# Optimization experiments

Hardware: AMD Instinct MI355X
Metric: run time of the kernel (lower is better)

The kernel has to match this reference:

```python
import jax, jax.numpy as jnp
import numpy as np

B, L, D, H, NB = 8, 256, 128, 4, 2
HD = D // H
N_ITEMS, TIME_SPAN = 50000, 256
EPS = 1e-8
NEG = -(2.0 ** 32) + 1.0  # torch uses -2**32+1 padding value


def _ln(x, g, b):
    m = jnp.mean(x, -1, keepdims=True)
    v = jnp.mean((x - m) ** 2, -1, keepdims=True)
    return (x - m) / jnp.sqrt(v + EPS) * g + b


def setup_inputs() -> dict:
    ks = iter(jax.random.split(jax.random.key(0), 40))

    def nrm(shape, s=0.02):
        return jax.random.normal(next(ks), shape, jnp.float32) * s

    inp = {
        "user_ids": jax.random.randint(next(ks), (B,), 0, 1000),
        "log_seqs": jax.random.randint(next(ks), (B, L), 0, N_ITEMS + 1),
        "time_matrices": jax.random.randint(next(ks), (B, L, L), 0, TIME_SPAN + 1),
        "pos_seqs": jax.random.randint(next(ks), (B, L), 1, N_ITEMS + 1),
        "neg_seqs": jax.random.randint(next(ks), (B, L), 1, N_ITEMS + 1),
    }
    inp["item_emb"] = nrm((N_ITEMS + 1, D)).at[0].set(0.0)  # padding_idx=0
    inp["posK_emb"] = nrm((L, D))
    inp["posV_emb"] = nrm((L, D))
    inp["timeK_emb"] = nrm((TIME_SPAN + 1, D))
    inp["timeV_emb"] = nrm((TIME_SPAN + 1, D))
    inp["ln1_g"] = jnp.ones((NB, D)); inp["ln1_b"] = jnp.zeros((NB, D))
    inp["Wq"] = nrm((NB, D, D)); inp["bq"] = jnp.zeros((NB, D))
    inp["Wk"] = nrm((NB, D, D)); inp["bk"] = jnp.zeros((NB, D))
    inp["Wv"] = nrm((NB, D, D)); inp["bv"] = jnp.zeros((NB, D))
    inp["ln2_g"] = jnp.ones((NB, D)); inp["ln2_b"] = jnp.zeros((NB, D))
    inp["W1"] = nrm((NB, D, D)); inp["b1"] = jnp.zeros((NB, D))
    inp["W2"] = nrm((NB, D, D)); inp["b2"] = jnp.zeros((NB, D))
    inp["lnf_g"] = jnp.ones((D,)); inp["lnf_b"] = jnp.zeros((D,))
    return inp


def reference(user_ids, log_seqs, time_matrices, pos_seqs, neg_seqs,
              item_emb, posK_emb, posV_emb, timeK_emb, timeV_emb,
              ln1_g, ln1_b, Wq, bq, Wk, bk, Wv, bv, ln2_g, ln2_b,
              W1, b1, W2, b2, lnf_g, lnf_b):
    # dropout layers are identity in eval mode
    seqs = item_emb[log_seqs] * jnp.sqrt(jnp.float32(D))          # [B,L,D]
    tK = timeK_emb[time_matrices].reshape(B, L, L, H, HD)          # [B,Lq,Lk,H,hd]
    tV = timeV_emb[time_matrices].reshape(B, L, L, H, HD)
    pad = log_seqs == 0                                            # [B,L]
    seqs = seqs * (~pad)[..., None]
    causal = jnp.triu(jnp.ones((L, L), bool), 1)                   # ~tril -> masked
    # time_mask masks by QUERY position (matches torch unsqueeze(-1).expand)
    mask = pad[:, None, :, None] | causal[None, None]              # [B,1,Lq,Lk]
    posKh = posK_emb.reshape(L, H, HD)
    posVh = posV_emb.reshape(L, H, HD)
    for i in range(NB):
        q_in = _ln(seqs, ln1_g[i], ln1_b[i])
        Qh = (q_in @ Wq[i] + bq[i]).reshape(B, L, H, HD).transpose(0, 2, 1, 3)
        Kh = (seqs @ Wk[i] + bk[i]).reshape(B, L, H, HD).transpose(0, 2, 1, 3)
        Vh = (seqs @ Wv[i] + bv[i]).reshape(B, L, H, HD).transpose(0, 2, 1, 3)
        scores = jnp.einsum("bhqd,bhkd->bhqk", Qh, Kh)
        scores = scores + jnp.einsum("bhqd,khd->bhqk", Qh, posKh)
        scores = scores + jnp.einsum("bqkhd,bhqd->bhqk", tK, Qh)
        scores = scores / jnp.sqrt(jnp.float32(HD))
        scores = jnp.where(mask, NEG, scores)
        A = jax.nn.softmax(scores, axis=-1)                        # [B,H,Lq,Lk]
        out = jnp.einsum("bhqk,bhkd->bhqd", A, Vh)
        out = out + jnp.einsum("bhqk,khd->bhqd", A, posVh)
        out = out + jnp.einsum("bhqk,bqkhd->bhqd", A, tV)
        out = out.transpose(0, 2, 1, 3).reshape(B, L, D)
        seqs = q_in + out                                          # residual on Q
        seqs = _ln(seqs, ln2_g[i], ln2_b[i])
        h = jax.nn.relu(seqs @ W1[i] + b1[i])                      # conv1d k=1 == linear
        seqs = seqs + (h @ W2[i] + b2[i])
        seqs = seqs * (~pad)[..., None]
    feats = _ln(seqs, lnf_g, lnf_b)
    pos_logits = jnp.sum(feats * item_emb[pos_seqs], -1)           # [B,L]
    neg_logits = jnp.sum(feats * item_emb[neg_seqs], -1)
    return (pos_logits, neg_logits)
```

## Files before the change

kernel.cpp:

```cpp
#include <hip/hip_runtime.h>
#include <hip/hip_bf16.h>

#define L_ 256
#define H_ 4
#define ROWS 2048
#define NEGV (-4294967295.0f)

typedef unsigned short us16;

__device__ __forceinline__ float us2f(us16 u){ return __uint_as_float(((unsigned)u)<<16); }
__device__ __forceinline__ us16 f2us(float f){ __hip_bfloat16 h=__float2bfloat16(f); return *(us16*)&h; }

struct KArgs {
    const int *log_seqs, *tmat, *pos_seqs, *neg_seqs;
    const float *item_emb, *posK, *posV, *timeK, *timeV;
    const float *ln1g, *ln1b, *bq, *bk, *bv, *ln2g, *ln2b, *b1, *b2, *lnfg, *lnfb;
    const float *Wq, *Wk, *Wv, *W1, *W2;
    float *qin0, *qin1, *out;
    us16 *wsW, *tmK, *tmV, *Qb0, *Kb0, *Vb0, *Qb1, *Kb1, *Vb1;
};

__device__ __forceinline__ void stage_w(const us16* __restrict__ Wg, us16* sW, int tid){
    const uint4* src=(const uint4*)Wg;
    uint4* dst=(uint4*)sW;
    #pragma unroll
    for(int j=0;j<8;j++) dst[j*256+tid]=src[j*256+tid];
}

__device__ __forceinline__ void ln_rows(float* sA,
        const float* __restrict__ g, const float* __restrict__ b,
        float* qin_out, int r0, int tid){
    int r=tid>>5, l=tid&31;
    float* x=sA+r*128;
    float x0=x[l],x1=x[l+32],x2=x[l+64],x3=x[l+96];
    float s=x0+x1+x2+x3;
    #pragma unroll
    for(int o=16;o;o>>=1) s+=__shfl_xor(s,o,64);
    float m=s*(1.f/128.f);
    float d0=x0-m,d1=x1-m,d2=x2-m,d3=x3-m;
    float v=d0*d0+d1*d1+d2*d2+d3*d3;
    #pragma unroll
    for(int o=16;o;o>>=1) v+=__shfl_xor(v,o,64);
    float rstd=rsqrtf(v*(1.f/128.f)+1e-8f);
    float y0=d0*rstd*g[l]+b[l];
    float y1=d1*rstd*g[l+32]+b[l+32];
    float y2=d2*rstd*g[l+64]+b[l+64];
    float y3=d3*rstd*g[l+96]+b[l+96];
    x[l]=y0; x[l+32]=y1; x[l+64]=y2; x[l+96]=y3;
    if(qin_out){
        float* q=qin_out+(size_t)(r0+r)*128;
        q[l]=y0; q[l+32]=y1; q[l+64]=y2; q[l+96]=y3;
    }
}

__device__ __forceinline__ void gemm2x2(const float* A, const us16* sW,
        int ra, int rb, int c0, float* acc){
    float a00=0,a01=0,a10=0,a11=0;
    const float* Ar=A+ra*128;
    const float* Br=A+rb*128;
    #pragma unroll 8
    for(int k=0;k<128;k++){
        ushort2 wp=*(const ushort2*)(sW+k*128+c0);
        float w0=us2f(wp.x), w1=us2f(wp.y);
        float x0=Ar[k], x1=Br[k];
        a00=fmaf(x0,w0,a00); a01=fmaf(x0,w1,a01);
        a10=fmaf(x1,w0,a10); a11=fmaf(x1,w1,a11);
    }
    acc[0]=a00; acc[1]=a01; acc[2]=a10; acc[3]=a11;
}

__global__ __launch_bounds__(256) void k_pre(KArgs a){
    __shared__ __align__(16) char smem[36864];
    int tid=threadIdx.x, bid=blockIdx.x;
    if(bid<768){
        us16* sW=(us16*)smem;
        float* sA=(float*)(smem+32768);
        int m=bid>>8, rg=bid&255, r0=rg*8;
        {
            int rl=tid>>5, c4=tid&31;
            int id=a.log_seqs[r0+rl];
            float4 v=((const float4*)a.item_emb)[id*32+c4];
            float sc = id? 11.3137085f : 0.f;
            v.x*=sc; v.y*=sc; v.z*=sc; v.w*=sc;
            ((float4*)sA)[tid]=v;
        }
        const float* Wsrc=(m==0)?a.Wq:(m==1)?a.Wk:a.Wv;
        {
            const float4* src=(const float4*)Wsrc;
            ushort4* dst=(ushort4*)sW;
            #pragma unroll
            for(int j=0;j<16;j++){
                float4 w=src[j*256+tid];
                ushort4 o; o.x=f2us(w.x);o.y=f2us(w.y);o.z=f2us(w.z);o.w=f2us(w.w);
                dst[j*256+tid]=o;
            }
        }
        __syncthreads();
        if(m==0){ ln_rows(sA, a.ln1g, a.ln1b, a.qin0, r0, tid); __syncthreads(); }
        int cp=tid&63, rp=tid>>6, c0=2*cp, ra=2*rp, rb=ra+1;
        float acc[4];
        gemm2x2(sA,sW,ra,rb,c0,acc);
        if(m==0){
            float b0v=a.bq[c0], b1v=a.bq[c0+1];
            ushort2 s0; s0.x=f2us(acc[0]+b0v); s0.y=f2us(acc[1]+b1v);
            ushort2 s1; s1.x=f2us(acc[2]+b0v); s1.y=f2us(acc[3]+b1v);
            *(ushort2*)(a.Qb0+(size_t)(r0+ra)*128+c0)=s0;
            *(ushort2*)(a.Qb0+(size_t)(r0+rb)*128+c0)=s1;
        } else {
            const float* bb=(m==1)?a.bk:a.bv;
            const float* pp=(m==1)?a.posK:a.posV;
            us16* Oo=(m==1)?a.Kb0:a.Vb0;
            int qa=(r0+ra)&255, qb2=(r0+rb)&255;
            float b0v=bb[c0], b1v=bb[c0+1];
            ushort2 s0; s0.x=f2us(acc[0]+b0v+pp[qa*128+c0]);  s0.y=f2us(acc[1]+b1v+pp[qa*128+c0+1]);
            ushort2 s1; s1.x=f2us(acc[2]+b0v+pp[qb2*128+c0]); s1.y=f2us(acc[3]+b1v+pp[qb2*128+c0+1]);
            *(ushort2*)(Oo+(size_t)(r0+ra)*128+c0)=s0;
            *(ushort2*)(Oo+(size_t)(r0+rb)*128+c0)=s1;
        }
    } else if(bid<880){
        int j=bid-768; int m=j>>4; int idx=(j&15)*256+tid;
        const float* base;
        switch(m){
            case 0: base=a.W1; break;        case 1: base=a.W2; break;
            case 2: base=a.Wq+16384; break;  case 3: base=a.Wk+16384; break;
            case 4: base=a.Wv+16384; break;  case 5: base=a.W1+16384; break;
            default: base=a.W2+16384; break;
        }
        float4 v=((const float4*)base)[idx];
        ushort4 o; o.x=f2us(v.x);o.y=f2us(v.y);o.z=f2us(v.z);o.w=f2us(v.w);
        ((ushort4*)(a.wsW+(size_t)m*16384))[idx]=o;
    } else {
        int gi=(bid-880)*256+tid;
        if(gi<8224){
            float4 v=((const float4*)a.timeK)[gi];
            ushort4 o; o.x=f2us(v.x);o.y=f2us(v.y);o.z=f2us(v.z);o.w=f2us(v.w);
            ((ushort4*)a.tmK)[gi]=o;
        } else if(gi<16448){
            int g2=gi-8224;
            float4 v=((const float4*)a.timeV)[g2];
            ushort4 o; o.x=f2us(v.x);o.y=f2us(v.y);o.z=f2us(v.z);o.w=f2us(v.w);
            ((ushort4*)a.tmV)[g2]=o;
        }
    }
}

__global__ __launch_bounds__(256,4) void k_blk(KArgs a, int layer){
    __shared__ __align__(16) char smem[36864];
    float* sQ  =(float*)smem;
    float* sS  =(float*)(smem+1024);
    int*   sTM =(int*)  (smem+9216);
    float* sPr =(float*)(smem+11264);
    float* sRed=(float*)(smem+19456);
    float* sRed2=(float*)(smem+19472);
    us16*  sW  =(us16*) smem;
    float* sX  =(float*)(smem+32768);
    float* sH  =(float*)(smem+33792);
    float* sY  =(float*)(smem+34816);
    float* sRB =(float*)(smem+35840);

    int tid=threadIdx.x, bid=blockIdx.x;
    int b=bid>>7, p=bid&127;
    int q1=p, q2=255-p, b0=b*L_;
    int r1=b0+q1, r2=b0+q2;
    bool pad1=a.log_seqs[r1]==0, pad2=a.log_seqs[r2]==0;
    const us16* Qb = layer? a.Qb1:a.Qb0;
    const us16* Kb = layer? a.Kb1:a.Kb0;
    const us16* Vb = layer? a.Vb1:a.Vb0;
    const float* qin = layer? a.qin1:a.qin0;
    const float scale=0.17677669529663687f;
    if(tid<128) sQ[tid]=us2f(Qb[(size_t)r1*128+tid])*scale;
    else        sQ[tid]=us2f(Qb[(size_t)r2*128+(tid-128)])*scale;
    int k=tid;
    int tm1=a.tmat[(size_t)r1*L_+k], tm2=a.tmat[(size_t)r2*L_+k];
    sTM[k]=tm1; sTM[256+k]=tm2;
    __syncthreads();

    {
        const uint4* K4=(const uint4*)(Kb+(size_t)(b0+k)*128);
        #pragma unroll
        for(int i2=0;i2<2;i2++){
            int qq=i2?q2:q1; bool pad=i2?pad2:pad1;
            int tm=i2?tm2:tm1;
            bool act=(k<=qq)&&!pad;
            float acc[4]={0.f,0.f,0.f,0.f};
            if(act){
                const uint4* T4=(const uint4*)(a.tmK+(size_t)tm*128);
                const float4* Q4=(const float4*)(sQ+i2*128);
                #pragma unroll
                for(int c=0;c<16;c++){
                    uint4 kv=K4[c]; uint4 tv=T4[c];
                    float4 qa=Q4[2*c], qb=Q4[2*c+1];
                    const us16* ku=(const us16*)&kv;
                    const us16* tu=(const us16*)&tv;
                    acc[c>>2]+= qa.x*(us2f(ku[0])+us2f(tu[0]))
                              + qa.y*(us2f(ku[1])+us2f(tu[1]))
                              + qa.z*(us2f(ku[2])+us2f(tu[2]))
                              + qa.w*(us2f(ku[3])+us2f(tu[3]))
                              + qb.x*(us2f(ku[4])+us2f(tu[4]))
                              + qb.y*(us2f(ku[5])+us2f(tu[5]))
                              + qb.z*(us2f(ku[6])+us2f(tu[6]))
                              + qb.w*(us2f(ku[7])+us2f(tu[7]));
                }
            }
            #pragma unroll
            for(int h=0;h<H_;h++) sS[(i2*4+h)*256+k]= act? acc[h]:NEGV;
        }
    }
    __syncthreads();

    {
        int h=tid>>6, lane=tid&63;
        #pragma unroll
        for(int i2=0;i2<2;i2++){
            float* row=sS+(i2*4+h)*256;
            float v0=row[lane],v1=row[lane+64],v2=row[lane+128],v3=row[lane+192];
            float mm=fmaxf(fmaxf(v0,v1),fmaxf(v2,v3));
            #pragma unroll
            for(int o=32;o;o>>=1) mm=fmaxf(mm,__shfl_xor(mm,o,64));
            float e0=__expf(v0-mm),e1=__expf(v1-mm),e2=__expf(v2-mm),e3=__expf(v3-mm);
            float ss=e0+e1+e2+e3;
            #pragma unroll
            for(int o=32;o;o>>=1) ss+=__shfl_xor(ss,o,64);
            float inv=1.f/ss;
            row[lane]=e0*inv; row[lane+64]=e1*inv; row[lane+128]=e2*inv; row[lane+192]=e3*inv;
        }
    }
    __syncthreads();

    {
        int i2=tid>>7, s8=(tid>>4)&7, dq=tid&15;
        int qq=i2?q2:q1; bool pad=i2?pad2:pad1;
        int kend=pad?L_:qq+1;
        int k0=s8*32;
        int kmax=kend-k0; kmax=kmax<0?0:(kmax>32?32:kmax);
        const float* row=sS+(i2*4+(dq>>2))*256;
        const int* tmrow=sTM+i2*256;
        float a0=0,a1=0,a2=0,a3=0,a4=0,a5=0,a6=0,a7=0;
        for(int kk=0;kk<kmax;kk++){
            int kx=k0+kk;
            float aa=row[kx];
            int tmk=tmrow[kx];
            uint4 v4=((const uint4*)(Vb+(size_t)(b0+kx)*128))[dq];
            uint4 t4=((const uint4*)(a.tmV+(size_t)tmk*128))[dq];
            const us16* vu=(const us16*)&v4;
            const us16* tu=(const us16*)&t4;
            a0=fmaf(aa,us2f(vu[0])+us2f(tu[0]),a0);
            a1=fmaf(aa,us2f(vu[1])+us2f(tu[1]),a1);
            a2=fmaf(aa,us2f(vu[2])+us2f(tu[2]),a2);
            a3=fmaf(aa,us2f(vu[3])+us2f(tu[3]),a3);
            a4=fmaf(aa,us2f(vu[4])+us2f(tu[4]),a4);
            a5=fmaf(aa,us2f(vu[5])+us2f(tu[5]),a5);
            a6=fmaf(aa,us2f(vu[6])+us2f(tu[6]),a6);
            a7=fmaf(aa,us2f(vu[7])+us2f(tu[7]),a7);
        }
        float* dst=sPr+(i2*8+s8)*128+dq*8;
        ((float4*)dst)[0]=make_float4(a0,a1,a2,a3);
        ((float4*)dst)[1]=make_float4(a4,a5,a6,a7);
    }
    __syncthreads();

    int ii=tid>>7, l=tid&127;
    bool padown = ii? pad2:pad1;
    int rr = ii? r2:r1;
    int qown = ii? q2:q1;
    {
        float v=qin[(size_t)rr*128+l];
        #pragma unroll
        for(int sl=0;sl<8;sl++) v+=sPr[(ii*8+sl)*128+l];
        float s=v;
        #pragma unroll
        for(int o=32;o;o>>=1) s+=__shfl_xor(s,o,64);
        if((tid&63)==0) sRed[ii*2+((tid>>6)&1)]=s;
        __syncthreads();
        float m=(sRed[ii*2]+sRed[ii*2+1])*(1.f/128.f);
        float d=v-m;
        float vv=d*d;
        #pragma unroll
        for(int o=32;o;o>>=1) vv+=__shfl_xor(vv,o,64);
        if((tid&63)==0) sRed2[ii*2+((tid>>6)&1)]=vv;
        __syncthreads();
        float rstd=rsqrtf((sRed2[ii*2]+sRed2[ii*2+1])*(1.f/128.f)+1e-8f);
        float y=d*rstd*a.ln2g[layer*128+l]+a.ln2b[layer*128+l];
        __syncthreads();
        sX[ii*128+l]=y;
    }
    __syncthreads();

    int cc=l;
    stage_w(a.wsW+(size_t)(layer?5:0)*16384, sW, tid);
    __syncthreads();
    {
        const float* xr=sX+ii*128;
        float h=0;
        #pragma unroll 16
        for(int k2=0;k2<128;k2++) h=fmaf(xr[k2],us2f(sW[k2*128+cc]),h);
        h=fmaxf(h+a.b1[layer*128+cc],0.f);
        __syncthreads();
        sH[ii*128+cc]=h;
    }
    __syncthreads();
    stage_w(a.wsW+(size_t)(layer?6:1)*16384, sW, tid);
    __syncthreads();
    float f;
    {
        const float* hr=sH+ii*128;
        float acc=0;
        #pragma unroll 16
        for(int k2=0;k2<128;k2++) acc=fmaf(hr[k2],us2f(sW[k2*128+cc]),acc);
        f=acc+a.b2[layer*128+cc]+sX[ii*128+cc];
        if(padown) f=0.f;
    }
    __syncthreads();

    if(layer==0){
        sY[ii*128+cc]=f;
        float s=f;
        #pragma unroll
        for(int o=32;o;o>>=1) s+=__shfl_xor(s,o,64);
        if((tid&63)==0) sRB[ii*2+((tid>>6)&1)]=s;
        __syncthreads();
        float m=(sRB[ii*2]+sRB[ii*2+1])*(1.f/128.f);
        float d=f-m;
        float vv=d*d;
        #pragma unroll
        for(int o=32;o;o>>=1) vv+=__shfl_xor(vv,o,64);
        if((tid&63)==0) sRB[4+ii*2+((tid>>6)&1)]=vv;
        __syncthreads();
        float rstd=rsqrtf((sRB[4+ii*2]+sRB[5+ii*2])*(1.f/128.f)+1e-8f);
        float y1=d*rstd*a.ln1g[128+cc]+a.ln1b[128+cc];
        a.qin1[(size_t)rr*128+cc]=y1;
        sX[ii*128+cc]=y1;
        __syncthreads();
        stage_w(a.wsW+(size_t)2*16384, sW, tid);
        __syncthreads();
        {
            const float* xr=sX+ii*128;
            float acc=0;
            #pragma unroll 16
            for(int k2=0;k2<128;k2++) acc=fmaf(xr[k2],us2f(sW[k2*128+cc]),acc);
            acc+=a.bq[128+cc];
            a.Qb1[(size_t)rr*128+cc]=f2us(acc);
        }
        __syncthreads();
        stage_w(a.wsW+(size_t)3*16384, sW, tid);
        __syncthreads();
        {
            const float* yr=sY+ii*128;
            float acc=0;
            #pragma unroll 16
            for(int k2=0;k2<128;k2++) acc=fmaf(yr[k2],us2f(sW[k2*128+cc]),acc);
            acc+=a.bk[128+cc]+a.posK[qown*128+cc];
            a.Kb1[(size_t)rr*128+cc]=f2us(acc);
        }
        __syncthreads();
        stage_w(a.wsW+(size_t)4*16384, sW, tid);
        __syncthreads();
        {
            const float* yr=sY+ii*128;
            float acc=0;
            #pragma unroll 16
            for(int k2=0;k2<128;k2++) acc=fmaf(yr[k2],us2f(sW[k2*128+cc]),acc);
            acc+=a.bv[128+cc]+a.posV[qown*128+cc];
            a.Vb1[(size_t)rr*128+cc]=f2us(acc);
        }
    } else {
        float s=f;
        #pragma unroll
        for(int o=32;o;o>>=1) s+=__shfl_xor(s,o,64);
        if((tid&63)==0) sRB[ii*2+((tid>>6)&1)]=s;
        __syncthreads();
        float m=(sRB[ii*2]+sRB[ii*2+1])*(1.f/128.f);
        float d=f-m;
        float vv=d*d;
        #pragma unroll
        for(int o=32;o;o>>=1) vv+=__shfl_xor(vv,o,64);
        if((tid&63)==0) sRB[4+ii*2+((tid>>6)&1)]=vv;
        __syncthreads();
        float rstd=rsqrtf((sRB[4+ii*2]+sRB[5+ii*2])*(1.f/128.f)+1e-8f);
        sX[ii*128+cc]=d*rstd*a.lnfg[cc]+a.lnfb[cc];
        __syncthreads();
        int w=tid>>6, lane=tid&63;
        int rowi=w>>1, neg=w&1;
        int rg = rowi? r2:r1;
        int id = neg? a.neg_seqs[rg] : a.pos_seqs[rg];
        const float* e=a.item_emb+(size_t)id*128;
        float s2 = sX[rowi*128+lane]*e[lane] + sX[rowi*128+lane+64]*e[lane+64];
        #pragma unroll
        for(int o=32;o;o>>=1) s2+=__shfl_xor(s2,o,64);
        if(lane==0) a.out[neg*ROWS+rg]=s2;
    }
}

extern "C" void kernel_launch(void* const* d_in, const int* in_sizes, int n_in,
                              void* d_out, int out_size, void* d_ws, size_t ws_size,
                              hipStream_t stream) {
    KArgs a;
    a.log_seqs=(const int*)d_in[1];
    a.tmat    =(const int*)d_in[2];
    a.pos_seqs=(const int*)d_in[3];
    a.neg_seqs=(const int*)d_in[4];
    a.item_emb=(const float*)d_in[5];
    a.posK =(const float*)d_in[6];
    a.posV =(const float*)d_in[7];
    a.timeK=(const float*)d_in[8];
    a.timeV=(const float*)d_in[9];
    a.ln1g=(const float*)d_in[10];
    a.ln1b=(const float*)d_in[11];
    a.Wq=(const float*)d_in[12];
    a.bq=(const float*)d_in[13];
    a.Wk=(const float*)d_in[14];
    a.bk=(const float*)d_in[15];
    a.Wv=(const float*)d_in[16];
    a.bv=(const float*)d_in[17];
    a.ln2g=(const float*)d_in[18];
    a.ln2b=(const float*)d_in[19];
    a.W1=(const float*)d_in[20];
    a.b1=(const float*)d_in[21];
    a.W2=(const float*)d_in[22];
    a.b2=(const float*)d_in[23];
    a.lnfg=(const float*)d_in[24];
    a.lnfb=(const float*)d_in[25];

    const size_t MB=1u<<20;
    char* w=(char*)d_ws;
    a.qin0=(float*)(w+0*MB);
    a.qin1=(float*)(w+1*MB);
    a.Qb0 =(us16*) (w+2*MB);
    a.Kb0 =(us16*) (w+2*MB+512*1024);
    a.Vb0 =(us16*) (w+3*MB);
    a.Qb1 =(us16*) (w+3*MB+512*1024);
    a.Kb1 =(us16*) (w+4*MB);
    a.Vb1 =(us16*) (w+4*MB+512*1024);
    a.wsW =(us16*) (w+5*MB);
    a.tmK =(us16*) (w+5*MB+256*1024);
    a.tmV =(us16*) (w+5*MB+384*1024);
    a.out =(float*)d_out;

    k_pre<<<946,256,0,stream>>>(a);
    k_blk<<<1024,256,0,stream>>>(a,0);
    k_blk<<<1024,256,0,stream>>>(a,1);
}
```

Measured before the change: 212.8 us.

## Precompute Q·timeK table per query and read transposed weights directly from global

Rather than gathering a timeK row for every (q,k) pair, each block computes dot products of its two queries with all 257 time embeddings into a shared table, then looks up that table when building scores. This swaps 256 gathers per query for 257 dense dot products. The small MLP and QKV GEMVs now read weights pre-transposed into column-major bf16 straight from global/L2, with no staging through LDS, which removes several barriers. Shared memory drops to 32KB and launch bounds go to 5 blocks per CU. The transposed writes in the pre-kernel become scattered stores.

```diff
diff --git a/kernel.cpp b/kernel.cpp
--- a/kernel.cpp
+++ b/kernel.cpp
@@ -17,15 +17,8 @@
     const float *ln1g, *ln1b, *bq, *bk, *bv, *ln2g, *ln2b, *b1, *b2, *lnfg, *lnfb;
     const float *Wq, *Wk, *Wv, *W1, *W2;
     float *qin0, *qin1, *out;
-    us16 *wsW, *tmK, *tmV, *Qb0, *Kb0, *Vb0, *Qb1, *Kb1, *Vb1;
+    us16 *wsWT, *tmK, *tmV, *Qb0, *Kb0, *Vb0, *Qb1, *Kb1, *Vb1;
 };
-
-__device__ __forceinline__ void stage_w(const us16* __restrict__ Wg, us16* sW, int tid){
-    const uint4* src=(const uint4*)Wg;
-    uint4* dst=(uint4*)sW;
-    #pragma unroll
-    for(int j=0;j<8;j++) dst[j*256+tid]=src[j*256+tid];
-}
 
 __device__ __forceinline__ void ln_rows(float* sA,
         const float* __restrict__ g, const float* __restrict__ b,
@@ -69,6 +62,20 @@
     acc[0]=a00; acc[1]=a01; acc[2]=a10; acc[3]=a11;
 }
 
+__device__ __forceinline__ float gemv_wt(const us16* __restrict__ wt, const float* x){
+    float acc=0;
+    const uint4* W4=(const uint4*)wt;
+    #pragma unroll
+    for(int c=0;c<16;c++){
+        uint4 wv=W4[c];
+        const us16* wu=(const us16*)&wv;
+        const float* xx=x+c*8;
+        acc += xx[0]*us2f(wu[0])+xx[1]*us2f(wu[1])+xx[2]*us2f(wu[2])+xx[3]*us2f(wu[3])
+             + xx[4]*us2f(wu[4])+xx[5]*us2f(wu[5])+xx[6]*us2f(wu[6])+xx[7]*us2f(wu[7]);
+    }
+    return acc;
+}
+
 __global__ __launch_bounds__(256) void k_pre(KArgs a){
     __shared__ __align__(16) char smem[36864];
     int tid=threadIdx.x, bid=blockIdx.x;
@@ -127,8 +134,13 @@
             default: base=a.W2+16384; break;
         }
         float4 v=((const float4*)base)[idx];
-        ushort4 o; o.x=f2us(v.x);o.y=f2us(v.y);o.z=f2us(v.z);o.w=f2us(v.w);
-        ((ushort4*)(a.wsW+(size_t)m*16384))[idx]=o;
+        int kRow = idx>>5;
+        int c0 = (idx&31)*4;
+        us16* dst = a.wsWT + (size_t)m*16384;
+        dst[(size_t)(c0+0)*128 + kRow]=f2us(v.x);
+        dst[(size_t)(c0+1)*128 + kRow]=f2us(v.y);
+        dst[(size_t)(c0+2)*128 + kRow]=f2us(v.z);
+        dst[(size_t)(c0+3)*128 + kRow]=f2us(v.w);
     } else {
         int gi=(bid-880)*256+tid;
         if(gi<8224){
@@ -144,19 +156,19 @@
     }
 }
 
-__global__ __launch_bounds__(256,4) void k_blk(KArgs a, int layer){
-    __shared__ __align__(16) char smem[36864];
+__global__ __launch_bounds__(256,5) void k_blk(KArgs a, int layer){
+    __shared__ __align__(16) char smem[32768];
     float* sQ  =(float*)smem;
     float* sS  =(float*)(smem+1024);
     int*   sTM =(int*)  (smem+9216);
     float* sPr =(float*)(smem+11264);
-    float* sRed=(float*)(smem+19456);
-    float* sRed2=(float*)(smem+19472);
-    us16*  sW  =(us16*) smem;
-    float* sX  =(float*)(smem+32768);
-    float* sH  =(float*)(smem+33792);
-    float* sY  =(float*)(smem+34816);
-    float* sRB =(float*)(smem+35840);
+    float* sDQ =(float*)(smem+19456);
+    float* sRed=(float*)(smem+27680);
+    float* sRed2=(float*)(smem+27696);
+    float* sX  =(float*)(smem+28672);
+    float* sH  =(float*)(smem+29696);
+    float* sY  =(float*)(smem+30720);
+    float* sRB =(float*)(smem+31744);
 
     int tid=threadIdx.x, bid=blockIdx.x;
     int b=bid>>7, p=bid&127;
@@ -175,35 +187,47 @@
     sTM[k]=tm1; sTM[256+k]=tm2;
     __syncthreads();
 
+    for(int j=tid;j<514;j+=256){
+        int i2 = j>=257; int t = j - i2*257;
+        const uint4* T4=(const uint4*)(a.tmK+(size_t)t*128);
+        const float* Qs = sQ + i2*128;
+        float acc[4]={0.f,0.f,0.f,0.f};
+        #pragma unroll
+        for(int c=0;c<16;c++){
+            uint4 tv=T4[c];
+            const us16* tu=(const us16*)&tv;
+            const float* qq=Qs+c*8;
+            acc[c>>2] += qq[0]*us2f(tu[0])+qq[1]*us2f(tu[1])
+                       + qq[2]*us2f(tu[2])+qq[3]*us2f(tu[3])
+                       + qq[4]*us2f(tu[4])+qq[5]*us2f(tu[5])
+                       + qq[6]*us2f(tu[6])+qq[7]*us2f(tu[7]);
+        }
+        #pragma unroll
+        for(int h=0;h<H_;h++) sDQ[(i2*4+h)*257+t]=acc[h];
+    }
+    __syncthreads();
+
     {
         const uint4* K4=(const uint4*)(Kb+(size_t)(b0+k)*128);
-        #pragma unroll
-        for(int i2=0;i2<2;i2++){
-            int qq=i2?q2:q1; bool pad=i2?pad2:pad1;
-            int tm=i2?tm2:tm1;
-            bool act=(k<=qq)&&!pad;
-            float acc[4]={0.f,0.f,0.f,0.f};
-            if(act){
-                const uint4* T4=(const uint4*)(a.tmK+(size_t)tm*128);
-                const float4* Q4=(const float4*)(sQ+i2*128);
-                #pragma unroll
-                for(int c=0;c<16;c++){
-                    uint4 kv=K4[c]; uint4 tv=T4[c];
-                    float4 qa=Q4[2*c], qb=Q4[2*c+1];
-                    const us16* ku=(const us16*)&kv;
-                    const us16* tu=(const us16*)&tv;
-                    acc[c>>2]+= qa.x*(us2f(ku[0])+us2f(tu[0]))
-                              + qa.y*(us2f(ku[1])+us2f(tu[1]))
-                              + qa.z*(us2f(ku[2])+us2f(tu[2]))
-                              + qa.w*(us2f(ku[3])+us2f(tu[3]))
-                              + qb.x*(us2f(ku[4])+us2f(tu[4]))
-                              + qb.y*(us2f(ku[5])+us2f(tu[5]))
-                              + qb.z*(us2f(ku[6])+us2f(tu[6]))
-                              + qb.w*(us2f(ku[7])+us2f(tu[7]));
-                }
-            }
-            #pragma unroll
-            for(int h=0;h<H_;h++) sS[(i2*4+h)*256+k]= act? acc[h]:NEGV;
+        float accA[4]={0.f,0.f,0.f,0.f}, accB[4]={0.f,0.f,0.f,0.f};
+        #pragma unroll
+        for(int c=0;c<16;c++){
+            uint4 kv=K4[c];
+            const us16* ku=(const us16*)&kv;
+            float kf0=us2f(ku[0]),kf1=us2f(ku[1]),kf2=us2f(ku[2]),kf3=us2f(ku[3]);
+            float kf4=us2f(ku[4]),kf5=us2f(ku[5]),kf6=us2f(ku[6]),kf7=us2f(ku[7]);
+            const float* qa=sQ+c*8;
+            const float* qb=sQ+128+c*8;
+            accA[c>>2] += qa[0]*kf0+qa[1]*kf1+qa[2]*kf2+qa[3]*kf3
+                        + qa[4]*kf4+qa[5]*kf5+qa[6]*kf6+qa[7]*kf7;
+            accB[c>>2] += qb[0]*kf0+qb[1]*kf1+qb[2]*kf2+qb[3]*kf3
+                        + qb[4]*kf4+qb[5]*kf5+qb[6]*kf6+qb[7]*kf7;
+        }
+        bool act1=(k<=q1)&&!pad1, act2=(k<=q2)&&!pad2;
+        #pragma unroll
+        for(int h=0;h<H_;h++){
+            sS[h*256+k]     = act1? accA[h]+sDQ[h*257+tm1]     : NEGV;
+            sS[(4+h)*256+k] = act2? accB[h]+sDQ[(4+h)*257+tm2] : NEGV;
         }
     }
     __syncthreads();
@@ -280,37 +304,25 @@
         if((tid&63)==0) sRed2[ii*2+((tid>>6)&1)]=vv;
         __syncthreads();
         float rstd=rsqrtf((sRed2[ii*2]+sRed2[ii*2+1])*(1.f/128.f)+1e-8f);
-        float y=d*rstd*a.ln2g[layer*128+l]+a.ln2b[layer*128+l];
-        __syncthreads();
-        sX[ii*128+l]=y;
+        sX[ii*128+l]=d*rstd*a.ln2g[layer*128+l]+a.ln2b[layer*128+l];
     }
     __syncthreads();
 
     int cc=l;
-    stage_w(a.wsW+(size_t)(layer?5:0)*16384, sW, tid);
-    __syncthreads();
-    {
-        const float* xr=sX+ii*128;
-        float h=0;
-        #pragma unroll 16
-        for(int k2=0;k2<128;k2++) h=fmaf(xr[k2],us2f(sW[k2*128+cc]),h);
-        h=fmaxf(h+a.b1[layer*128+cc],0.f);
-        __syncthreads();
+    const us16* WT1 = a.wsWT + (size_t)(layer?5:0)*16384;
+    const us16* WT2 = a.wsWT + (size_t)(layer?6:1)*16384;
+    {
+        float h = gemv_wt(WT1 + (size_t)cc*128, sX+ii*128);
+        h = fmaxf(h + a.b1[layer*128+cc], 0.f);
         sH[ii*128+cc]=h;
     }
     __syncthreads();
-    stage_w(a.wsW+(size_t)(layer?6:1)*16384, sW, tid);
-    __syncthreads();
     float f;
     {
-        const float* hr=sH+ii*128;
-        float acc=0;
-        #pragma unroll 16
-        for(int k2=0;k2<128;k2++) acc=fmaf(hr[k2],us2f(sW[k2*128+cc]),acc);
-        f=acc+a.b2[layer*128+cc]+sX[ii*128+cc];
+        f = gemv_wt(WT2 + (size_t)cc*128, sH+ii*128)
+          + a.b2[layer*128+cc] + sX[ii*128+cc];
         if(padown) f=0.f;
     }
-    __syncthreads();
 
     if(layer==0){
         sY[ii*128+cc]=f;
@@ -331,37 +343,17 @@
         a.qin1[(size_t)rr*128+cc]=y1;
         sX[ii*128+cc]=y1;
         __syncthreads();
-        stage_w(a.wsW+(size_t)2*16384, sW, tid);
-        __syncthreads();
         {
-            const float* xr=sX+ii*128;
-            float acc=0;
-            #pragma unroll 16
-            for(int k2=0;k2<128;k2++) acc=fmaf(xr[k2],us2f(sW[k2*128+cc]),acc);
-            acc+=a.bq[128+cc];
-            a.Qb1[(size_t)rr*128+cc]=f2us(acc);
-        }
-        __syncthreads();
-        stage_w(a.wsW+(size_t)3*16384, sW, tid);
-        __syncthreads();
+            float acc = gemv_wt(a.wsWT + (size_t)2*16384 + (size_t)cc*128, sX+ii*128);
+            a.Qb1[(size_t)rr*128+cc]=f2us(acc + a.bq[128+cc]);
+        }
         {
-            const float* yr=sY+ii*128;
-            float acc=0;
-            #pragma unroll 16
-            for(int k2=0;k2<128;k2++) acc=fmaf(yr[k2],us2f(sW[k2*128+cc]),acc);
-            acc+=a.bk[128+cc]+a.posK[qown*128+cc];
-            a.Kb1[(size_t)rr*128+cc]=f2us(acc);
-        }
-        __syncthreads();
-        stage_w(a.wsW+(size_t)4*16384, sW, tid);
-        __syncthreads();
+            float acc = gemv_wt(a.wsWT + (size_t)3*16384 + (size_t)cc*128, sY+ii*128);
+            a.Kb1[(size_t)rr*128+cc]=f2us(acc + a.bk[128+cc] + a.posK[qown*128+cc]);
+        }
         {
-            const float* yr=sY+ii*128;
-            float acc=0;
-            #pragma unroll 16
-            for(int k2=0;k2<128;k2++) acc=fmaf(yr[k2],us2f(sW[k2*128+cc]),acc);
-            acc+=a.bv[128+cc]+a.posV[qown*128+cc];
-            a.Vb1[(size_t)rr*128+cc]=f2us(acc);
+            float acc = gemv_wt(a.wsWT + (size_t)4*16384 + (size_t)cc*128, sY+ii*128);
+            a.Vb1[(size_t)rr*128+cc]=f2us(acc + a.bv[128+cc] + a.posV[qown*128+cc]);
         }
     } else {
         float s=f;
@@ -431,7 +423,7 @@
     a.Qb1 =(us16*) (w+3*MB+512*1024);
     a.Kb1 =(us16*) (w+4*MB);
     a.Vb1 =(us16*) (w+4*MB+512*1024);
-    a.wsW =(us16*) (w+5*MB);
+    a.wsWT=(us16*) (w+5*MB);
     a.tmK =(us16*) (w+5*MB+256*1024);
     a.tmV =(us16*) (w+5*MB+384*1024);
     a.out =(float*)d_out;
```

New measurement: 406.0 us. 1.91x slower.

## Double k_blk threads to 512 and split work across query rows and K halves

Applied to the files above, without the earlier changes.

Each block of k_blk now runs 512 threads. The score phase gives each query row its own thread half, the AV phase splits keys into 16 slices, and each 128x128 GEMV splits its K dimension across two thread halves, with partial sums reduced through shared memory. Time indices are stored as 16-bit values to free shared memory. The aim is more parallelism and latency hiding per block. The cost is extra barriers, idle threads in the LayerNorm sections, and larger shared-memory use, which may reduce occupancy.

```diff
diff --git a/kernel.cpp b/kernel.cpp
--- a/kernel.cpp
+++ b/kernel.cpp
@@ -19,13 +19,6 @@
     float *qin0, *qin1, *out;
     us16 *wsW, *tmK, *tmV, *Qb0, *Kb0, *Vb0, *Qb1, *Kb1, *Vb1;
 };
-
-__device__ __forceinline__ void stage_w(const us16* __restrict__ Wg, us16* sW, int tid){
-    const uint4* src=(const uint4*)Wg;
-    uint4* dst=(uint4*)sW;
-    #pragma unroll
-    for(int j=0;j<8;j++) dst[j*256+tid]=src[j*256+tid];
-}
 
 __device__ __forceinline__ void ln_rows(float* sA,
         const float* __restrict__ g, const float* __restrict__ b,
@@ -144,19 +137,36 @@
     }
 }
 
-__global__ __launch_bounds__(256,4) void k_blk(KArgs a, int layer){
-    __shared__ __align__(16) char smem[36864];
+__device__ __forceinline__ void stage_w512(const us16* __restrict__ Wg, us16* sW, int tid){
+    const uint4* src=(const uint4*)Wg;
+    uint4* dst=(uint4*)sW;
+    #pragma unroll
+    for(int j=0;j<4;j++) dst[j*512+tid]=src[j*512+tid];
+}
+
+__device__ __forceinline__ float gemv_half(const us16* sW, const float* x, int kh, int cc){
+    float acc=0;
+    int k0=kh*64;
+    #pragma unroll 16
+    for(int j=0;j<64;j++)
+        acc=fmaf(x[k0+j], us2f(sW[(size_t)(k0+j)*128+cc]), acc);
+    return acc;
+}
+
+__global__ __launch_bounds__(512,6) void k_blk(KArgs a, int layer){
+    __shared__ __align__(16) char smem[38912];
     float* sQ  =(float*)smem;
     float* sS  =(float*)(smem+1024);
-    int*   sTM =(int*)  (smem+9216);
-    float* sPr =(float*)(smem+11264);
-    float* sRed=(float*)(smem+19456);
-    float* sRed2=(float*)(smem+19472);
-    us16*  sW  =(us16*) smem;
+    us16*  sTMu=(us16*)(smem+9216);
+    float* sPr =(float*)(smem+10240);
+    float* sRed=(float*)(smem+26624);
+    float* sRed2=(float*)(smem+26640);
+    us16*  sW  =(us16*)smem;
     float* sX  =(float*)(smem+32768);
     float* sH  =(float*)(smem+33792);
     float* sY  =(float*)(smem+34816);
-    float* sRB =(float*)(smem+35840);
+    float* sPart=(float*)(smem+35840);
+    float* sRB =(float*)(smem+37888);
 
     int tid=threadIdx.x, bid=blockIdx.x;
     int b=bid>>7, p=bid&127;
@@ -168,73 +178,69 @@
     const us16* Vb = layer? a.Vb1:a.Vb0;
     const float* qin = layer? a.qin1:a.qin0;
     const float scale=0.17677669529663687f;
-    if(tid<128) sQ[tid]=us2f(Qb[(size_t)r1*128+tid])*scale;
-    else        sQ[tid]=us2f(Qb[(size_t)r2*128+(tid-128)])*scale;
-    int k=tid;
-    int tm1=a.tmat[(size_t)r1*L_+k], tm2=a.tmat[(size_t)r2*L_+k];
-    sTM[k]=tm1; sTM[256+k]=tm2;
+    if(tid<256){
+        int i2=tid>>7, l=tid&127;
+        sQ[tid]=us2f(Qb[(size_t)(i2?r2:r1)*128+l])*scale;
+    }
+    int i2g=tid>>8, kg=tid&255;
+    int rg_ = i2g? r2:r1;
+    int tmg = a.tmat[(size_t)rg_*L_+kg];
+    sTMu[i2g*256+kg]=(us16)tmg;
     __syncthreads();
 
     {
-        const uint4* K4=(const uint4*)(Kb+(size_t)(b0+k)*128);
-        #pragma unroll
-        for(int i2=0;i2<2;i2++){
-            int qq=i2?q2:q1; bool pad=i2?pad2:pad1;
-            int tm=i2?tm2:tm1;
-            bool act=(k<=qq)&&!pad;
-            float acc[4]={0.f,0.f,0.f,0.f};
-            if(act){
-                const uint4* T4=(const uint4*)(a.tmK+(size_t)tm*128);
-                const float4* Q4=(const float4*)(sQ+i2*128);
-                #pragma unroll
-                for(int c=0;c<16;c++){
-                    uint4 kv=K4[c]; uint4 tv=T4[c];
-                    float4 qa=Q4[2*c], qb=Q4[2*c+1];
-                    const us16* ku=(const us16*)&kv;
-                    const us16* tu=(const us16*)&tv;
-                    acc[c>>2]+= qa.x*(us2f(ku[0])+us2f(tu[0]))
-                              + qa.y*(us2f(ku[1])+us2f(tu[1]))
-                              + qa.z*(us2f(ku[2])+us2f(tu[2]))
-                              + qa.w*(us2f(ku[3])+us2f(tu[3]))
-                              + qb.x*(us2f(ku[4])+us2f(tu[4]))
-                              + qb.y*(us2f(ku[5])+us2f(tu[5]))
-                              + qb.z*(us2f(ku[6])+us2f(tu[6]))
-                              + qb.w*(us2f(ku[7])+us2f(tu[7]));
-                }
+        int qq = i2g? q2:q1; bool pad = i2g? pad2:pad1;
+        bool act=(kg<=qq)&&!pad;
+        float acc[4]={0.f,0.f,0.f,0.f};
+        if(act){
+            const uint4* K4=(const uint4*)(Kb+(size_t)(b0+kg)*128);
+            const uint4* T4=(const uint4*)(a.tmK+(size_t)tmg*128);
+            const float4* Q4=(const float4*)(sQ+i2g*128);
+            #pragma unroll 4
+            for(int c=0;c<16;c++){
+                uint4 kv=K4[c]; uint4 tv=T4[c];
+                float4 qa=Q4[2*c], qb=Q4[2*c+1];
+                const us16* ku=(const us16*)&kv;
+                const us16* tu=(const us16*)&tv;
+                acc[c>>2]+= qa.x*(us2f(ku[0])+us2f(tu[0]))
+                          + qa.y*(us2f(ku[1])+us2f(tu[1]))
+                          + qa.z*(us2f(ku[2])+us2f(tu[2]))
+                          + qa.w*(us2f(ku[3])+us2f(tu[3]))
+                          + qb.x*(us2f(ku[4])+us2f(tu[4]))
+                          + qb.y*(us2f(ku[5])+us2f(tu[5]))
+                          + qb.z*(us2f(ku[6])+us2f(tu[6]))
+                          + qb.w*(us2f(ku[7])+us2f(tu[7]));
             }
-            #pragma unroll
-            for(int h=0;h<H_;h++) sS[(i2*4+h)*256+k]= act? acc[h]:NEGV;
-        }
+        }
+        #pragma unroll
+        for(int h=0;h<H_;h++) sS[(i2g*4+h)*256+kg]= act? acc[h]:NEGV;
     }
     __syncthreads();
 
     {
-        int h=tid>>6, lane=tid&63;
-        #pragma unroll
-        for(int i2=0;i2<2;i2++){
-            float* row=sS+(i2*4+h)*256;
-            float v0=row[lane],v1=row[lane+64],v2=row[lane+128],v3=row[lane+192];
-            float mm=fmaxf(fmaxf(v0,v1),fmaxf(v2,v3));
-            #pragma unroll
-            for(int o=32;o;o>>=1) mm=fmaxf(mm,__shfl_xor(mm,o,64));
-            float e0=__expf(v0-mm),e1=__expf(v1-mm),e2=__expf(v2-mm),e3=__expf(v3-mm);
-            float ss=e0+e1+e2+e3;
-            #pragma unroll
-            for(int o=32;o;o>>=1) ss+=__shfl_xor(ss,o,64);
-            float inv=1.f/ss;
-            row[lane]=e0*inv; row[lane+64]=e1*inv; row[lane+128]=e2*inv; row[lane+192]=e3*inv;
-        }
+        int w=tid>>6, lane=tid&63;
+        float* row=sS+w*256;
+        float v0=row[lane],v1=row[lane+64],v2=row[lane+128],v3=row[lane+192];
+        float mm=fmaxf(fmaxf(v0,v1),fmaxf(v2,v3));
+        #pragma unroll
+        for(int o=32;o;o>>=1) mm=fmaxf(mm,__shfl_xor(mm,o,64));
+        float e0=__expf(v0-mm),e1=__expf(v1-mm),e2=__expf(v2-mm),e3=__expf(v3-mm);
+        float ss=e0+e1+e2+e3;
+        #pragma unroll
+        for(int o=32;o;o>>=1) ss+=__shfl_xor(ss,o,64);
+        float inv=1.f/ss;
+        row[lane]=e0*inv; row[lane+64]=e1*inv; row[lane+128]=e2*inv; row[lane+192]=e3*inv;
     }
     __syncthreads();
 
     {
-        int i2=tid>>7, s8=(tid>>4)&7, dq=tid&15;
+        int i2=tid>>8, s16=(tid>>4)&15, dq=tid&15;
         int qq=i2?q2:q1; bool pad=i2?pad2:pad1;
         int kend=pad?L_:qq+1;
-        int k0=s8*32;
-        int kmax=kend-k0; kmax=kmax<0?0:(kmax>32?32:kmax);
+        int k0=s16*16;
+        int kmax=kend-k0; kmax=kmax<0?0:(kmax>16?16:kmax);
         const float* row=sS+(i2*4+(dq>>2))*256;
-        const int* tmrow=sTM+i2*256;
+        const us16* tmrow=sTMu+i2*256;
         float a0=0,a1=0,a2=0,a3=0,a4=0,a5=0,a6=0,a7=0;
         for(int kk=0;kk<kmax;kk++){
             int kx=k0+kk;
@@ -253,20 +259,18 @@
             a6=fmaf(aa,us2f(vu[6])+us2f(tu[6]),a6);
             a7=fmaf(aa,us2f(vu[7])+us2f(tu[7]),a7);
         }
-        float* dst=sPr+(i2*8+s8)*128+dq*8;
+        float* dst=sPr+(i2*16+s16)*128+dq*8;
         ((float4*)dst)[0]=make_float4(a0,a1,a2,a3);
         ((float4*)dst)[1]=make_float4(a4,a5,a6,a7);
     }
     __syncthreads();
 
-    int ii=tid>>7, l=tid&127;
-    bool padown = ii? pad2:pad1;
-    int rr = ii? r2:r1;
-    int qown = ii? q2:q1;
-    {
+    if(tid<256){
+        int ii=tid>>7, l=tid&127;
+        int rr = ii? r2:r1;
         float v=qin[(size_t)rr*128+l];
         #pragma unroll
-        for(int sl=0;sl<8;sl++) v+=sPr[(ii*8+sl)*128+l];
+        for(int sl=0;sl<16;sl++) v+=sPr[(ii*16+sl)*128+l];
         float s=v;
         #pragma unroll
         for(int o=32;o;o>>=1) s+=__shfl_xor(s,o,64);
@@ -280,114 +284,99 @@
         if((tid&63)==0) sRed2[ii*2+((tid>>6)&1)]=vv;
         __syncthreads();
         float rstd=rsqrtf((sRed2[ii*2]+sRed2[ii*2+1])*(1.f/128.f)+1e-8f);
-        float y=d*rstd*a.ln2g[layer*128+l]+a.ln2b[layer*128+l];
-        __syncthreads();
-        sX[ii*128+l]=y;
-    }
-    __syncthreads();
-
-    int cc=l;
-    stage_w(a.wsW+(size_t)(layer?5:0)*16384, sW, tid);
-    __syncthreads();
-    {
-        const float* xr=sX+ii*128;
-        float h=0;
-        #pragma unroll 16
-        for(int k2=0;k2<128;k2++) h=fmaf(xr[k2],us2f(sW[k2*128+cc]),h);
-        h=fmaxf(h+a.b1[layer*128+cc],0.f);
-        __syncthreads();
-        sH[ii*128+cc]=h;
-    }
-    __syncthreads();
-    stage_w(a.wsW+(size_t)(layer?6:1)*16384, sW, tid);
-    __syncthreads();
-    float f;
-    {
-        const float* hr=sH+ii*128;
-        float acc=0;
-        #pragma unroll 16
-        for(int k2=0;k2<128;k2++) acc=fmaf(hr[k2],us2f(sW[k2*128+cc]),acc);
-        f=acc+a.b2[layer*128+cc]+sX[ii*128+cc];
+        sX[ii*128+l]=d*rstd*a.ln2g[layer*128+l]+a.ln2b[layer*128+l];
+    } else { __syncthreads(); __syncthreads(); }
+    __syncthreads();
+
+    int out=tid&255, kh=tid>>8, ii=out>>7, cc=out&127;
+    int rr = ii? r2:r1;
+    int qown = ii? q2:q1;
+    bool padown = ii? pad2:pad1;
+
+    stage_w512(a.wsW+(size_t)(layer?5:0)*16384, sW, tid);
+    __syncthreads();
+    sPart[tid]=gemv_half(sW, sX+ii*128, kh, cc);
+    __syncthreads();
+    if(tid<256) sH[out]=fmaxf(sPart[tid]+sPart[tid+256]+a.b1[layer*128+cc],0.f);
+    __syncthreads();
+    stage_w512(a.wsW+(size_t)(layer?6:1)*16384, sW, tid);
+    __syncthreads();
+    sPart[tid]=gemv_half(sW, sH+ii*128, kh, cc);
+    __syncthreads();
+    float f=0.f;
+    if(tid<256){
+        f=sPart[tid]+sPart[tid+256]+a.b2[layer*128+cc]+sX[out];
         if(padown) f=0.f;
+        sY[out]=f;
     }
     __syncthreads();
 
     if(layer==0){
-        sY[ii*128+cc]=f;
-        float s=f;
-        #pragma unroll
-        for(int o=32;o;o>>=1) s+=__shfl_xor(s,o,64);
-        if((tid&63)==0) sRB[ii*2+((tid>>6)&1)]=s;
-        __syncthreads();
-        float m=(sRB[ii*2]+sRB[ii*2+1])*(1.f/128.f);
-        float d=f-m;
-        float vv=d*d;
-        #pragma unroll
-        for(int o=32;o;o>>=1) vv+=__shfl_xor(vv,o,64);
-        if((tid&63)==0) sRB[4+ii*2+((tid>>6)&1)]=vv;
-        __syncthreads();
-        float rstd=rsqrtf((sRB[4+ii*2]+sRB[5+ii*2])*(1.f/128.f)+1e-8f);
-        float y1=d*rstd*a.ln1g[128+cc]+a.ln1b[128+cc];
-        a.qin1[(size_t)rr*128+cc]=y1;
-        sX[ii*128+cc]=y1;
-        __syncthreads();
-        stage_w(a.wsW+(size_t)2*16384, sW, tid);
-        __syncthreads();
-        {
-            const float* xr=sX+ii*128;
-            float acc=0;
-            #pragma unroll 16
-            for(int k2=0;k2<128;k2++) acc=fmaf(xr[k2],us2f(sW[k2*128+cc]),acc);
-            acc+=a.bq[128+cc];
-            a.Qb1[(size_t)rr*128+cc]=f2us(acc);
-        }
-        __syncthreads();
-        stage_w(a.wsW+(size_t)3*16384, sW, tid);
-        __syncthreads();
-        {
-            const float* yr=sY+ii*128;
-            float acc=0;
-            #pragma unroll 16
-            for(int k2=0;k2<128;k2++) acc=fmaf(yr[k2],us2f(sW[k2*128+cc]),acc);
-            acc+=a.bk[128+cc]+a.posK[qown*128+cc];
-            a.Kb1[(size_t)rr*128+cc]=f2us(acc);
-        }
-        __syncthreads();
-        stage_w(a.wsW+(size_t)4*16384, sW, tid);
-        __syncthreads();
-        {
-            const float* yr=sY+ii*128;
-            float acc=0;
-            #pragma unroll 16
-            for(int k2=0;k2<128;k2++) acc=fmaf(yr[k2],us2f(sW[k2*128+cc]),acc);
-            acc+=a.bv[128+cc]+a.posV[qown*128+cc];
-            a.Vb1[(size_t)rr*128+cc]=f2us(acc);
-        }
+        if(tid<256){
+            float s=f;
+            #pragma unroll
+            for(int o=32;o;o>>=1) s+=__shfl_xor(s,o,64);
+            if((tid&63)==0) sRB[ii*2+((tid>>6)&1)]=s;
+            __syncthreads();
+            float m=(sRB[ii*2]+sRB[ii*2+1])*(1.f/128.f);
+            float d=f-m;
+            float vv=d*d;
+            #pragma unroll
+            for(int o=32;o;o>>=1) vv+=__shfl_xor(vv,o,64);
+            if((tid&63)==0) sRB[4+ii*2+((tid>>6)&1)]=vv;
+            __syncthreads();
+            float rstd=rsqrtf((sRB[4+ii*2]+sRB[5+ii*2])*(1.f/128.f)+1e-8f);
+            float y1=d*rstd*a.ln1g[128+cc]+a.ln1b[128+cc];
+            a.qin1[(size_t)rr*128+cc]=y1;
+            sX[out]=y1;
+        } else { __syncthreads(); __syncthreads(); }
+        __syncthreads();
+        stage_w512(a.wsW+(size_t)2*16384, sW, tid);
+        __syncthreads();
+        sPart[tid]=gemv_half(sW, sX+ii*128, kh, cc);
+        __syncthreads();
+        if(tid<256) a.Qb1[(size_t)rr*128+cc]=f2us(sPart[tid]+sPart[tid+256]+a.bq[128+cc]);
+        __syncthreads();
+        stage_w512(a.wsW+(size_t)3*16384, sW, tid);
+        __syncthreads();
+        sPart[tid]=gemv_half(sW, sY+ii*128, kh, cc);
+        __syncthreads();
+        if(tid<256) a.Kb1[(size_t)rr*128+cc]=f2us(sPart[tid]+sPart[tid+256]+a.bk[128+cc]+a.posK[qown*128+cc]);
+        __syncthreads();
+        stage_w512(a.wsW+(size_t)4*16384, sW, tid);
+        __syncthreads();
+        sPart[tid]=gemv_half(sW, sY+ii*128, kh, cc);
+        __syncthreads();
+        if(tid<256) a.Vb1[(size_t)rr*128+cc]=f2us(sPart[tid]+sPart[tid+256]+a.bv[128+cc]+a.posV[qown*128+cc]);
     } else {
-        float s=f;
-        #pragma unroll
-        for(int o=32;o;o>>=1) s+=__shfl_xor(s,o,64);
-        if((tid&63)==0) sRB[ii*2+((tid>>6)&1)]=s;
-        __syncthreads();
-        float m=(sRB[ii*2]+sRB[ii*2+1])*(1.f/128.f);
-        float d=f-m;
-        float vv=d*d;
-        #pragma unroll
-        for(int o=32;o;o>>=1) vv+=__shfl_xor(vv,o,64);
-        if((tid&63)==0) sRB[4+ii*2+((tid>>6)&1)]=vv;
-        __syncthreads();
-        float rstd=rsqrtf((sRB[4+ii*2]+sRB[5+ii*2])*(1.f/128.f)+1e-8f);
-        sX[ii*128+cc]=d*rstd*a.lnfg[cc]+a.lnfb[cc];
+        if(tid<256){
+            float s=f;
+            #pragma unroll
+            for(int o=32;o;o>>=1) s+=__shfl_xor(s,o,64);
+            if((tid&63)==0) sRB[ii*2+((tid>>6)&1)]=s;
+            __syncthreads();
+            float m=(sRB[ii*2]+sRB[ii*2+1])*(1.f/128.f);
+            float d=f-m;
+            float vv=d*d;
+            #pragma unroll
+            for(int o=32;o;o>>=1) vv+=__shfl_xor(vv,o,64);
+            if((tid&63)==0) sRB[4+ii*2+((tid>>6)&1)]=vv;
+            __syncthreads();
+            float rstd=rsqrtf((sRB[4+ii*2]+sRB[5+ii*2])*(1.f/128.f)+1e-8f);
+            sX[out]=d*rstd*a.lnfg[cc]+a.lnfb[cc];
+        } else { __syncthreads(); __syncthreads(); }
         __syncthreads();
         int w=tid>>6, lane=tid&63;
-        int rowi=w>>1, neg=w&1;
-        int rg = rowi? r2:r1;
-        int id = neg? a.neg_seqs[rg] : a.pos_seqs[rg];
-        const float* e=a.item_emb+(size_t)id*128;
-        float s2 = sX[rowi*128+lane]*e[lane] + sX[rowi*128+lane+64]*e[lane+64];
-        #pragma unroll
-        for(int o=32;o;o>>=1) s2+=__shfl_xor(s2,o,64);
-        if(lane==0) a.out[neg*ROWS+rg]=s2;
+        if(w<4){
+            int rowi=w>>1, neg=w&1;
+            int rg = rowi? r2:r1;
+            int id = neg? a.neg_seqs[rg] : a.pos_seqs[rg];
+            const float* e=a.item_emb+(size_t)id*128;
+            float s2 = sX[rowi*128+lane]*e[lane] + sX[rowi*128+lane+64]*e[lane+64];
+            #pragma unroll
+            for(int o=32;o;o>>=1) s2+=__shfl_xor(s2,o,64);
+            if(lane==0) a.out[neg*ROWS+rg]=s2;
+        }
     }
 }
 
@@ -437,6 +426,6 @@
     a.out =(float*)d_out;
 
     k_pre<<<946,256,0,stream>>>(a);
-    k_blk<<<1024,256,0,stream>>>(a,0);
-    k_blk<<<1024,256,0,stream>>>(a,1);
-}
+    k_blk<<<1024,512,0,stream>>>(a,0);
+    k_blk<<<1024,512,0,stream>>>(a,1);
+}
```

Result: slower. 231.3 us (+8.7%).
